# Kernel optimization log

Measured on AMD Instinct MI355X. Metric: run time of the kernel, lower is better.

## Reference

```python
import jax, jax.numpy as jnp
import numpy as np

N = 100_000      # nodes
E = 1_600_000    # edges (avg degree 16)
D_IN = 64        # node feature dim
H = 128          # hidden
E_IN = 64        # edge feature dim
C = 8            # num classes
EPS = 1e-5       # BatchNorm eps


def setup_inputs() -> dict:
    key = jax.random.key(0)
    ks = jax.random.split(key, 22)
    w = lambda k, shape: jax.random.normal(k, shape, dtype=jnp.float32) * 0.05
    return {
        "x_nodes": jax.random.normal(ks[0], (N, D_IN), dtype=jnp.float32),
        "e_feat": jax.random.normal(ks[1], (E, E_IN), dtype=jnp.float32),
        # SAGE layer 1 (fc_self, fc_neigh, bias)
        "Ws1": w(ks[2], (D_IN, H)), "Wn1": w(ks[3], (D_IN, H)), "b1": w(ks[4], (H,)),
        "g1": 1.0 + 0.1 * jax.random.normal(ks[5], (H,), dtype=jnp.float32),
        "bt1": 0.1 * jax.random.normal(ks[6], (H,), dtype=jnp.float32),
        # SAGE layer 2
        "Ws2": w(ks[7], (H, H)), "Wn2": w(ks[8], (H, H)), "b2": w(ks[9], (H,)),
        "g2": 1.0 + 0.1 * jax.random.normal(ks[10], (H,), dtype=jnp.float32),
        "bt2": 0.1 * jax.random.normal(ks[11], (H,), dtype=jnp.float32),
        # Edge MLP
        "We1": w(ks[12], (2 * H + E_IN, H)), "be1": w(ks[13], (H,)),
        "We2": w(ks[14], (H, C)), "be2": w(ks[15], (C,)),
        # Graph structure (message-flow graph, reused for both layers) and pair graph
        "src": jax.random.randint(ks[16], (E,), 0, N, dtype=jnp.int32),
        "dst": jax.random.randint(ks[17], (E,), 0, N, dtype=jnp.int32),
        "u": jax.random.randint(ks[18], (E,), 0, N, dtype=jnp.int32),
        "v": jax.random.randint(ks[19], (E,), 0, N, dtype=jnp.int32),
    }


def _sage_mean(h, src, dst, inv_deg, Ws, Wn, b):
    # DGL SAGEConv('mean'): rst = fc_self(h_dst) + fc_neigh(mean_{in-neighbors} h_src) + bias
    agg = jax.ops.segment_sum(h[src], dst, num_segments=h.shape[0]) * inv_deg[:, None]
    return h @ Ws + agg @ Wn + b


def _bn_relu(h, gamma, beta):
    # BatchNorm1d (training-mode batch stats, biased variance) + ReLU
    mu = h.mean(axis=0)
    var = jnp.mean((h - mu) ** 2, axis=0)
    return jax.nn.relu((h - mu) * jax.lax.rsqrt(var + EPS) * gamma + beta)


def reference(x_nodes, e_feat, Ws1, Wn1, b1, g1, bt1, Ws2, Wn2, b2, g2, bt2,
              We1, be1, We2, be2, src, dst, u, v):
    n = x_nodes.shape[0]
    deg = jax.ops.segment_sum(jnp.ones_like(src, dtype=x_nodes.dtype), dst, num_segments=n)
    inv_deg = jnp.where(deg > 0, 1.0 / jnp.maximum(deg, 1.0), 0.0)  # zero-degree -> 0 (DGL mean)
    h = _bn_relu(_sage_mean(x_nodes, src, dst, inv_deg, Ws1, Wn1, b1), g1, bt1)
    h = _bn_relu(_sage_mean(h, src, dst, inv_deg, Ws2, Wn2, b2), g2, bt2)
    # edge head: gather endpoints, concat with edge features, MLP (dropout = eval identity)
    e_repr = jnp.concatenate([h[u], h[v], e_feat], axis=1)  # [E, 2H + E_IN]
    hid = jax.nn.relu(e_repr @ We1 + be1)
    return hid @ We2 + be2
```

## Files before the change

### kernel.cpp

```cpp
#include <hip/hip_runtime.h>

#define NN 100000
#define EE 1600000
constexpr float BN_EPS = 1e-5f;

typedef __attribute__((ext_vector_type(8))) short short8;
typedef __attribute__((ext_vector_type(4))) float f32x4;

__device__ __forceinline__ short f2bf(float f) {
    unsigned u = __float_as_uint(f);
    u += 0x7fff + ((u >> 16) & 1);
    return (short)(u >> 16);
}
__device__ __forceinline__ float bf2f(short s) {
    return __uint_as_float(((unsigned)(unsigned short)s) << 16);
}

typedef __attribute__((address_space(1))) const unsigned int guint;
typedef __attribute__((address_space(3))) unsigned int luint;
__device__ __forceinline__ void gload_lds16(const void* g, void* l) {
    __builtin_amdgcn_global_load_lds((guint*)g, (luint*)l, 16, 0, 0);
}

__global__ void k_count(const int* __restrict__ dst, int* __restrict__ cnt) {
    int e = blockIdx.x * 256 + threadIdx.x;
    if (e < EE) atomicAdd(&cnt[dst[e]], 1);
}

__global__ __launch_bounds__(1024) void k_scan(const int* __restrict__ cnt,
                                               int* __restrict__ offs,
                                               int* __restrict__ cursor,
                                               float* __restrict__ invd) {
    const int t = threadIdx.x, lane = t & 63, w = t >> 6;
    __shared__ int wsum[16], wexcl[16];
    __shared__ int carry_sh;
    if (t == 0) carry_sh = 0;
    __syncthreads();
    int ss = 0;
    for (int base = 0; base < NN; base += 1024) {
        int i = base + t;
        int v = (i < NN) ? cnt[i] : 0;
        int s = v;
#pragma unroll
        for (int d = 1; d < 64; d <<= 1) {
            int o = __shfl_up(s, d, 64);
            if (lane >= d) s += o;
        }
        if (lane == 63) wsum[w] = s;
        __syncthreads();
        if (t < 16) {
            int wv = wsum[t];
            ss = wv;
#pragma unroll
            for (int d = 1; d < 16; d <<= 1) {
                int o = __shfl_up(ss, d, 16);
                if (t >= d) ss += o;
            }
            wexcl[t] = ss - wv;
        }
        __syncthreads();
        int excl = (s - v) + wexcl[w];
        int c = carry_sh;
        if (i < NN) {
            int o = c + excl;
            offs[i] = o;
            cursor[i] = o;
            invd[i] = v > 0 ? 1.f / (float)v : 0.f;
        }
        __syncthreads();
        if (t == 15) carry_sh = c + ss;
        __syncthreads();
    }
    if (t == 0) offs[NN] = carry_sh;
}

__global__ void k_fill(const int* __restrict__ src, const int* __restrict__ dst,
                       int* __restrict__ cursor, int* __restrict__ eidsrc) {
    int e = blockIdx.x * 256 + threadIdx.x;
    if (e < EE) {
        int pos = atomicAdd(&cursor[dst[e]], 1);
        eidsrc[pos] = src[e];
    }
}

__global__ void k_f2bf(const float* __restrict__ in, short* __restrict__ out, int n8) {
    int i = blockIdx.x * 256 + threadIdx.x;
    if (i >= n8) return;
    float4 a = ((const float4*)in)[i * 2];
    float4 b = ((const float4*)in)[i * 2 + 1];
    short8 o;
    o[0] = f2bf(a.x); o[1] = f2bf(a.y); o[2] = f2bf(a.z); o[3] = f2bf(a.w);
    o[4] = f2bf(b.x); o[5] = f2bf(b.y); o[6] = f2bf(b.z); o[7] = f2bf(b.w);
    ((short8*)out)[i] = o;
}

template <int F>
__global__ __launch_bounds__(256) void k_gather_bf(
    const short* __restrict__ hbsrc, const int* __restrict__ offs,
    const int* __restrict__ eidsrc, const float* __restrict__ invd,
    short* __restrict__ aggb) {
    constexpr int G = F / 8;
    int gid = blockIdx.x * 256 + threadIdx.x;
    int node = gid / G;
    int sub = gid % G;
    if (node >= NN) return;
    int beg = offs[node], end = offs[node + 1];
    float iv = invd[node];
    float s[8] = {0.f, 0.f, 0.f, 0.f, 0.f, 0.f, 0.f, 0.f};
    const size_t co = (size_t)sub * 8;
    int p = beg;
    for (; p + 4 <= end; p += 4) {
        int i0 = eidsrc[p], i1 = eidsrc[p + 1], i2 = eidsrc[p + 2], i3 = eidsrc[p + 3];
        short8 r0 = *(const short8*)(hbsrc + (size_t)i0 * F + co);
        short8 r1 = *(const short8*)(hbsrc + (size_t)i1 * F + co);
        short8 r2 = *(const short8*)(hbsrc + (size_t)i2 * F + co);
        short8 r3 = *(const short8*)(hbsrc + (size_t)i3 * F + co);
#pragma unroll
        for (int j = 0; j < 8; ++j)
            s[j] += (bf2f(r0[j]) + bf2f(r1[j])) + (bf2f(r2[j]) + bf2f(r3[j]));
    }
    for (; p < end; ++p) {
        short8 r = *(const short8*)(hbsrc + (size_t)eidsrc[p] * F + co);
#pragma unroll
        for (int j = 0; j < 8; ++j) s[j] += bf2f(r[j]);
    }
    short8 o;
#pragma unroll
    for (int j = 0; j < 8; ++j) o[j] = f2bf(s[j] * iv);
    *(short8*)(aggb + (size_t)node * F + co) = o;
}

__device__ __forceinline__ void packW(const float* W, short* Wp, int local, int kbase) {
    int k = local >> 7, col = local & 127;
    int gk = k + kbase;
    int kc = gk >> 5, kw = gk & 31, bp = kw >> 3, j = kw & 7;
    int cb = col >> 4, n = col & 15;
    Wp[kc * 4096 + (cb * 64 + bp * 16 + n) * 8 + j] = f2bf(W[k * 128 + col]);
}

__global__ void k_pack_all(const float* __restrict__ We1, const float* __restrict__ Ws1,
                           const float* __restrict__ Wn1, const float* __restrict__ Ws2,
                           const float* __restrict__ Wn2, const float* __restrict__ We2,
                           short* __restrict__ Wp_e, short* __restrict__ Wp1,
                           short* __restrict__ Wp2, short* __restrict__ Wp2e) {
    int idx = blockIdx.x * 256 + threadIdx.x;
    if (idx < 40960) {
        packW(We1, Wp_e, idx, 0);
    } else if (idx < 49152) {
        packW(Ws1, Wp1, idx - 40960, 0);
    } else if (idx < 57344) {
        packW(Wn1, Wp1, idx - 49152, 64);
    } else if (idx < 73728) {
        packW(Ws2, Wp2, idx - 57344, 0);
    } else if (idx < 90112) {
        packW(Wn2, Wp2, idx - 73728, 128);
    } else if (idx < 92160) {
        int local = idx - 90112;
        int k = local >> 4, n = local & 15;
        float val = (n < 8) ? We2[k * 8 + n] : 0.f;
        int kc2 = k >> 5, kl = k & 31, bp = kl >> 3, j = kl & 7;
        Wp2e[(kc2 * 64 + bp * 16 + n) * 8 + j] = f2bf(val);
    }
}

template <int KC1, int KC2>
__global__ __launch_bounds__(256) void k_node_mfma(
    const short* __restrict__ A1, const short* __restrict__ A2,
    const short* __restrict__ Wp, const float* __restrict__ bias,
    float* __restrict__ outf, float* __restrict__ stats) {
    __shared__ __align__(16) short sbuf[16384];
    __shared__ float bs[128];
    __shared__ float reds[4][128], redss[4][128];
    const int t = threadIdx.x;
    if (t < 128) bs[t] = bias[t];
    const int rowbase = blockIdx.x * 128;
    const int lane = t & 63, w = t >> 6;
    const int fo = (lane >> 4) * 16 + (lane & 15);

    auto NSTAGE = [&](int kc, short* Ad, short* Bd) {
        const short* src;
        int kst, kloc;
        if (kc < KC1) { src = A1; kst = KC1 * 32; kloc = kc * 32; }
        else          { src = A2; kst = KC2 * 32; kloc = (kc - KC1) * 32; }
#pragma unroll
        for (int p = 0; p < 2; ++p) {
            int s = t + p * 256;
            int b = (s >> 4) & 3;
            int row = rowbase + ((s >> 6) << 4) + (s & 15);
            gload_lds16(src + (size_t)row * kst + kloc + b * 8, Ad + s * 8);
            gload_lds16(Wp + (size_t)kc * 4096 + s * 8, Bd + s * 8);
        }
    };

    f32x4 acc[2][8];
#pragma unroll
    for (int i = 0; i < 2; ++i)
#pragma unroll
        for (int j = 0; j < 8; ++j) acc[i][j] = (f32x4){0.f, 0.f, 0.f, 0.f};

    constexpr int KC = KC1 + KC2;
    NSTAGE(0, sbuf, sbuf + 4096);
    __syncthreads();
    for (int kc = 0; kc < KC; ++kc) {
        const int cur = kc & 1;
        short* Ac = sbuf + (cur ? 8192 : 0);
        short* Bc = Ac + 4096;
        if (kc + 1 < KC) {
            short* An = sbuf + (cur ? 0 : 8192);
            NSTAGE(kc + 1, An, An + 4096);
        }
        short8 a0 = *(const short8*)(Ac + (2 * w * 64 + fo) * 8);
        short8 a1 = *(const short8*)(Ac + ((2 * w + 1) * 64 + fo) * 8);
#pragma unroll
        for (int cb = 0; cb < 8; ++cb) {
            short8 bfr = *(const short8*)(Bc + (cb * 64 + fo) * 8);
            acc[0][cb] = __builtin_amdgcn_mfma_f32_16x16x32_bf16(a0, bfr, acc[0][cb], 0, 0, 0);
            acc[1][cb] = __builtin_amdgcn_mfma_f32_16x16x32_bf16(a1, bfr, acc[1][cb], 0, 0, 0);
        }
        __syncthreads();
    }

    float cs[8], css[8];
#pragma unroll
    for (int cb = 0; cb < 8; ++cb) { cs[cb] = 0.f; css[cb] = 0.f; }
#pragma unroll
    for (int rb2 = 0; rb2 < 2; ++rb2) {
        int rloc = 32 * w + rb2 * 16 + ((lane >> 4) << 2);
#pragma unroll
        for (int cb = 0; cb < 8; ++cb) {
            int col = cb * 16 + (lane & 15);
            float bb = bs[col];
#pragma unroll
            for (int i = 0; i < 4; ++i) {
                int row = rowbase + rloc + i;
                if (row < NN) {
                    float v = acc[rb2][cb][i] + bb;
                    outf[(size_t)row * 128 + col] = v;
                    cs[cb] += v;
                    css[cb] += v * v;
                }
            }
        }
    }
#pragma unroll
    for (int cb = 0; cb < 8; ++cb) {
        cs[cb] += __shfl_xor(cs[cb], 16);
        cs[cb] += __shfl_xor(cs[cb], 32);
        css[cb] += __shfl_xor(css[cb], 16);
        css[cb] += __shfl_xor(css[cb], 32);
    }
    if (lane < 16) {
#pragma unroll
        for (int cb = 0; cb < 8; ++cb) {
            reds[w][cb * 16 + lane] = cs[cb];
            redss[w][cb * 16 + lane] = css[cb];
        }
    }
    __syncthreads();
    if (t < 128) {
        atomicAdd(&stats[t], reds[0][t] + reds[1][t] + reds[2][t] + reds[3][t]);
    } else {
        int c = t - 128;
        atomicAdd(&stats[128 + c], redss[0][c] + redss[1][c] + redss[2][c] + redss[3][c]);
    }
}

__global__ void k_bnrelu_bf16(const float* __restrict__ h, const float* __restrict__ stats,
                              const float* __restrict__ g, const float* __restrict__ bt,
                              short* __restrict__ hb) {
    int gid = blockIdx.x * 256 + threadIdx.x;
    if (gid >= NN * 16) return;
    int c8 = gid & 15;
    float av[8], bv[8];
#pragma unroll
    for (int j = 0; j < 8; ++j) {
        int c = c8 * 8 + j;
        float mu = stats[c] * (1.f / NN);
        float var = stats[128 + c] * (1.f / NN) - mu * mu;
        float a = g[c] * rsqrtf(var + BN_EPS);
        av[j] = a;
        bv[j] = bt[c] - mu * a;
    }
    float4 v0 = reinterpret_cast<const float4*>(h)[gid * 2];
    float4 v1 = reinterpret_cast<const float4*>(h)[gid * 2 + 1];
    short8 o;
    o[0] = f2bf(fmaxf(fmaf(av[0], v0.x, bv[0]), 0.f));
    o[1] = f2bf(fmaxf(fmaf(av[1], v0.y, bv[1]), 0.f));
    o[2] = f2bf(fmaxf(fmaf(av[2], v0.z, bv[2]), 0.f));
    o[3] = f2bf(fmaxf(fmaf(av[3], v0.w, bv[3]), 0.f));
    o[4] = f2bf(fmaxf(fmaf(av[4], v1.x, bv[4]), 0.f));
    o[5] = f2bf(fmaxf(fmaf(av[5], v1.y, bv[5]), 0.f));
    o[6] = f2bf(fmaxf(fmaf(av[6], v1.z, bv[6]), 0.f));
    o[7] = f2bf(fmaxf(fmaf(av[7], v1.w, bv[7]), 0.f));
    reinterpret_cast<short8*>(hb)[gid] = o;
}

__global__ __launch_bounds__(256) void k_edge_mfma(
    const short* __restrict__ hb, const float* __restrict__ ef,
    const short* __restrict__ Wp, const short* __restrict__ Wp2e,
    const float* __restrict__ be1, const float* __restrict__ be2,
    const int* __restrict__ uu, const int* __restrict__ vv,
    float* __restrict__ out) {
    __shared__ __align__(16) short smem[17408];
    __shared__ float be1s[128];
    __shared__ int suv[256];
    const int t = threadIdx.x;
    const int eb = blockIdx.x * 128;
    if (t < 128) {
        suv[t] = uu[eb + t];
        suv[128 + t] = vv[eb + t];
        be1s[t] = be1[t];
    }
    const int lane = t & 63, w = t >> 6;
    const int fo = (lane >> 4) * 16 + (lane & 15);
    const int srow = t >> 1;
    const int sb0 = (t & 1) * 2;
    const int sslotbase = (srow >> 4) * 64 + (srow & 15);

    short8 b2f[4];
#pragma unroll
    for (int kc2 = 0; kc2 < 4; ++kc2)
        b2f[kc2] = *(const short8*)(Wp2e + (kc2 * 64 + fo) * 8);

    short8 efs[4];
    {
        const float* er = ef + (size_t)(eb + srow) * 64;
#pragma unroll
        for (int kcx = 0; kcx < 2; ++kcx)
#pragma unroll
            for (int pp = 0; pp < 2; ++pp) {
                int b = sb0 + pp;
                float4 f0 = *(const float4*)(er + kcx * 32 + b * 8);
                float4 f1 = *(const float4*)(er + kcx * 32 + b * 8 + 4);
                short8 v8;
                v8[0] = f2bf(f0.x); v8[1] = f2bf(f0.y);
                v8[2] = f2bf(f0.z); v8[3] = f2bf(f0.w);
                v8[4] = f2bf(f1.x); v8[5] = f2bf(f1.y);
                v8[6] = f2bf(f1.z); v8[7] = f2bf(f1.w);
                efs[kcx * 2 + pp] = v8;
            }
    }
    __syncthreads();

    auto STAGE = [&](int kc, short* Ad, short* Bd) {
        if (kc < 8) {
#pragma unroll
            for (int p = 0; p < 2; ++p) {
                int s = t + p * 256;
                int b = (s >> 4) & 3;
                int row = ((s >> 6) << 4) + (s & 15);
                const short* gsrc =
                    hb + (size_t)suv[(kc >= 4) * 128 + row] * 128 + (kc & 3) * 32 + b * 8;
                gload_lds16(gsrc, Ad + s * 8);
            }
        } else {
#pragma unroll
            for (int p = 0; p < 2; ++p)
                *(short8*)(Ad + (sslotbase + (sb0 + p) * 16) * 8) = efs[(kc - 8) * 2 + p];
        }
#pragma unroll
        for (int p = 0; p < 2; ++p) {
            int s = t + p * 256;
            gload_lds16(Wp + (size_t)kc * 4096 + s * 8, Bd + s * 8);
        }
    };

    f32x4 acc[2][8];
#pragma unroll
    for (int i = 0; i < 2; ++i)
#pragma unroll
        for (int j = 0; j < 8; ++j) acc[i][j] = (f32x4){0.f, 0.f, 0.f, 0.f};

    STAGE(0, smem, smem + 4096);
    __syncthreads();
    for (int kc = 0; kc < 10; ++kc) {
        const int cur = kc & 1;
        short* Ac = smem + (cur ? 8192 : 0);
        short* Bc = Ac + 4096;
        if (kc < 9) {
            short* An = smem + (cur ? 0 : 8192);
            STAGE(kc + 1, An, An + 4096);
        }
        short8 afr0 = *(const short8*)(Ac + (2 * w * 64 + fo) * 8);
        short8 afr1 = *(const short8*)(Ac + ((2 * w + 1) * 64 + fo) * 8);
#pragma unroll
        for (int cb = 0; cb < 8; ++cb) {
            short8 bfr = *(const short8*)(Bc + (cb * 64 + fo) * 8);
            acc[0][cb] = __builtin_amdgcn_mfma_f32_16x16x32_bf16(afr0, bfr, acc[0][cb], 0, 0, 0);
            acc[1][cb] = __builtin_amdgcn_mfma_f32_16x16x32_bf16(afr1, bfr, acc[1][cb], 0, 0, 0);
        }
        __syncthreads();
    }

    short* Hid = smem;
#pragma unroll
    for (int rb2 = 0; rb2 < 2; ++rb2)
#pragma unroll
        for (int cb = 0; cb < 8; ++cb) {
            int col = cb * 16 + (lane & 15);
            int rbase = 32 * w + rb2 * 16 + ((lane >> 4) << 2);
            float bb = be1s[col];
#pragma unroll
            for (int i = 0; i < 4; ++i)
                Hid[(rbase + i) * 136 + col] = f2bf(fmaxf(acc[rb2][cb][i] + bb, 0.f));
        }
    __syncthreads();

#pragma unroll
    for (int rf = 0; rf < 2; ++rf) {
        f32x4 a2 = (f32x4){0.f, 0.f, 0.f, 0.f};
        const int rbl = 32 * w + 16 * rf + (lane & 15);
#pragma unroll
        for (int kc2 = 0; kc2 < 4; ++kc2) {
            short8 af = *(const short8*)(Hid + rbl * 136 + kc2 * 32 + 8 * (lane >> 4));
            a2 = __builtin_amdgcn_mfma_f32_16x16x32_bf16(af, b2f[kc2], a2, 0, 0, 0);
        }
        int col = lane & 15;
        if (col < 8) {
            int r0 = eb + 32 * w + 16 * rf + 4 * (lane >> 4);
            float bb = be2[col];
#pragma unroll
            for (int i = 0; i < 4; ++i)
                out[(size_t)(r0 + i) * 8 + col] = a2[i] + bb;
        }
    }
}

extern "C" void kernel_launch(void* const* d_in, const int* in_sizes, int n_in,
                              void* d_out, int out_size, void* d_ws, size_t ws_size,
                              hipStream_t stream) {
    const float* x   = (const float*)d_in[0];
    const float* ef  = (const float*)d_in[1];
    const float* Ws1 = (const float*)d_in[2];
    const float* Wn1 = (const float*)d_in[3];
    const float* b1  = (const float*)d_in[4];
    const float* g1  = (const float*)d_in[5];
    const float* bt1 = (const float*)d_in[6];
    const float* Ws2 = (const float*)d_in[7];
    const float* Wn2 = (const float*)d_in[8];
    const float* b2  = (const float*)d_in[9];
    const float* g2  = (const float*)d_in[10];
    const float* bt2 = (const float*)d_in[11];
    const float* We1 = (const float*)d_in[12];
    const float* be1 = (const float*)d_in[13];
    const float* We2 = (const float*)d_in[14];
    const float* be2 = (const float*)d_in[15];
    const int* src = (const int*)d_in[16];
    const int* dst = (const int*)d_in[17];
    const int* u   = (const int*)d_in[18];
    const int* v   = (const int*)d_in[19];
    float* out = (float*)d_out;

    char* p = (char*)d_ws;
    auto take = [&](size_t bytes) {
        char* r = p;
        p += (bytes + 255) & ~(size_t)255;
        return r;
    };
    int* cnt     = (int*)take(NN * 4);
    float* stats = (float*)take(512 * 4);
    float* invd  = (float*)take(NN * 4);
    int* offs    = (int*)take((NN + 1) * 4);
    int* cursor  = (int*)take(NN * 4);
    int* eidsrc  = (int*)take((size_t)EE * 4);
    short* Wp_e  = (short*)take(320 * 128 * 2);
    short* Wp1   = (short*)take(128 * 128 * 2);
    short* Wp2   = (short*)take(256 * 128 * 2);
    short* Wp2e  = (short*)take(256 * 8 * 2);
    short* xb    = (short*)take((size_t)NN * 64 * 2);
    short* agg1b = (short*)take((size_t)NN * 64 * 2);
    short* h1b   = (short*)take((size_t)NN * 128 * 2);
    short* agg2b = (short*)take((size_t)NN * 128 * 2);
    take(65536);
    float* h1 = out;
    float* h2 = out;
    short* hb = xb;

    hipMemsetAsync(cnt, 0, ((char*)stats - (char*)cnt) + 512 * 4, stream);
    k_count<<<(EE + 255) / 256, 256, 0, stream>>>(dst, cnt);
    k_scan<<<1, 1024, 0, stream>>>(cnt, offs, cursor, invd);
    k_fill<<<(EE + 255) / 256, 256, 0, stream>>>(src, dst, cursor, eidsrc);
    k_pack_all<<<360, 256, 0, stream>>>(We1, Ws1, Wn1, Ws2, Wn2, We2, Wp_e, Wp1, Wp2, Wp2e);
    k_f2bf<<<(NN * 8 + 255) / 256, 256, 0, stream>>>(x, xb, NN * 8);

    k_gather_bf<64><<<(NN * 8 + 255) / 256, 256, 0, stream>>>(xb, offs, eidsrc, invd, agg1b);
    k_node_mfma<2, 2><<<(NN + 127) / 128, 256, 0, stream>>>(xb, agg1b, Wp1, b1, h1, stats);
    k_bnrelu_bf16<<<(NN * 16 + 255) / 256, 256, 0, stream>>>(h1, stats, g1, bt1, h1b);

    k_gather_bf<128><<<(NN * 16 + 255) / 256, 256, 0, stream>>>(h1b, offs, eidsrc, invd, agg2b);
    k_node_mfma<4, 4><<<(NN + 127) / 128, 256, 0, stream>>>(h1b, agg2b, Wp2, b2, h2, stats + 256);
    k_bnrelu_bf16<<<(NN * 16 + 255) / 256, 256, 0, stream>>>(h2, stats + 256, g2, bt2, hb);

    k_edge_mfma<<<EE / 128, 256, 0, stream>>>(hb, ef, Wp_e, Wp2e, be1, be2, u, v, out);
}
```

Baseline: 773.0 us.

## Parallelize degree scan, hoist BN coefficients to LDS, single-buffer edge MFMA

Replaces the single-block serial prefix scan over node degrees with a three-kernel reduce/base/final scan spread across many blocks, removing a long single-CU serial phase. BatchNorm scale and shift are now computed once per block into shared memory instead of per thread for eight channels. The edge MLP kernel drops double buffering and register prefetch of edge features, loading each K-chunk into a single LDS buffer and syncing before compute. This lowers register pressure but loses load/compute overlap.

Measured after the change: 662.0 us. 1.17x faster.

```diff
diff --git a/kernel.cpp b/kernel.cpp
--- a/kernel.cpp
+++ b/kernel.cpp
@@ -27,51 +27,70 @@
     if (e < EE) atomicAdd(&cnt[dst[e]], 1);
 }
 
-__global__ __launch_bounds__(1024) void k_scan(const int* __restrict__ cnt,
-                                               int* __restrict__ offs,
-                                               int* __restrict__ cursor,
-                                               float* __restrict__ invd) {
+__global__ __launch_bounds__(1024) void k_scan_part(const int* __restrict__ cnt,
+                                                    int* __restrict__ bsum) {
+    const int t = threadIdx.x, lane = t & 63, w = t >> 6;
+    int i = blockIdx.x * 1024 + t;
+    int v = (i < NN) ? cnt[i] : 0;
+#pragma unroll
+    for (int d = 1; d < 64; d <<= 1) v += __shfl_xor(v, d, 64);
+    __shared__ int ws[16];
+    if (lane == 0) ws[w] = v;
+    __syncthreads();
+    if (t == 0) {
+        int s = 0;
+#pragma unroll
+        for (int k = 0; k < 16; ++k) s += ws[k];
+        bsum[blockIdx.x] = s;
+    }
+}
+
+__global__ void k_scan_base(int* __restrict__ bsum, int* __restrict__ offs, int nb) {
+    if (threadIdx.x == 0) {
+        int run = 0;
+        for (int k = 0; k < nb; ++k) {
+            int v = bsum[k];
+            bsum[k] = run;
+            run += v;
+        }
+        offs[NN] = run;
+    }
+}
+
+__global__ __launch_bounds__(1024) void k_scan_final(const int* __restrict__ cnt,
+                                                     const int* __restrict__ bsum,
+                                                     int* __restrict__ offs,
+                                                     int* __restrict__ cursor,
+                                                     float* __restrict__ invd) {
     const int t = threadIdx.x, lane = t & 63, w = t >> 6;
     __shared__ int wsum[16], wexcl[16];
-    __shared__ int carry_sh;
-    if (t == 0) carry_sh = 0;
-    __syncthreads();
-    int ss = 0;
-    for (int base = 0; base < NN; base += 1024) {
-        int i = base + t;
-        int v = (i < NN) ? cnt[i] : 0;
-        int s = v;
-#pragma unroll
-        for (int d = 1; d < 64; d <<= 1) {
-            int o = __shfl_up(s, d, 64);
-            if (lane >= d) s += o;
-        }
-        if (lane == 63) wsum[w] = s;
-        __syncthreads();
-        if (t < 16) {
-            int wv = wsum[t];
-            ss = wv;
-#pragma unroll
-            for (int d = 1; d < 16; d <<= 1) {
-                int o = __shfl_up(ss, d, 16);
-                if (t >= d) ss += o;
-            }
-            wexcl[t] = ss - wv;
-        }
-        __syncthreads();
-        int excl = (s - v) + wexcl[w];
-        int c = carry_sh;
-        if (i < NN) {
-            int o = c + excl;
-            offs[i] = o;
-            cursor[i] = o;
-            invd[i] = v > 0 ? 1.f / (float)v : 0.f;
-        }
-        __syncthreads();
-        if (t == 15) carry_sh = c + ss;
-        __syncthreads();
-    }
-    if (t == 0) offs[NN] = carry_sh;
+    int i = blockIdx.x * 1024 + t;
+    int v = (i < NN) ? cnt[i] : 0;
+    int s = v;
+#pragma unroll
+    for (int d = 1; d < 64; d <<= 1) {
+        int o = __shfl_up(s, d, 64);
+        if (lane >= d) s += o;
+    }
+    if (lane == 63) wsum[w] = s;
+    __syncthreads();
+    if (t < 16) {
+        int wv = wsum[t];
+        int ss = wv;
+#pragma unroll
+        for (int d = 1; d < 16; d <<= 1) {
+            int o = __shfl_up(ss, d, 16);
+            if (t >= d) ss += o;
+        }
+        wexcl[t] = ss - wv;
+    }
+    __syncthreads();
+    if (i < NN) {
+        int o = bsum[blockIdx.x] + (s - v) + wexcl[w];
+        offs[i] = o;
+        cursor[i] = o;
+        invd[i] = v > 0 ? 1.f / (float)v : 0.f;
+    }
 }
 
 __global__ void k_fill(const int* __restrict__ src, const int* __restrict__ dst,
@@ -268,30 +287,30 @@
 __global__ void k_bnrelu_bf16(const float* __restrict__ h, const float* __restrict__ stats,
                               const float* __restrict__ g, const float* __restrict__ bt,
                               short* __restrict__ hb) {
-    int gid = blockIdx.x * 256 + threadIdx.x;
+    __shared__ float a_sh[128], b_sh[128];
+    const int t = threadIdx.x;
+    if (t < 128) {
+        float mu = stats[t] * (1.f / NN);
+        float var = stats[128 + t] * (1.f / NN) - mu * mu;
+        float a = g[t] * rsqrtf(var + BN_EPS);
+        a_sh[t] = a;
+        b_sh[t] = bt[t] - mu * a;
+    }
+    __syncthreads();
+    int gid = blockIdx.x * 256 + t;
     if (gid >= NN * 16) return;
-    int c8 = gid & 15;
-    float av[8], bv[8];
-#pragma unroll
-    for (int j = 0; j < 8; ++j) {
-        int c = c8 * 8 + j;
-        float mu = stats[c] * (1.f / NN);
-        float var = stats[128 + c] * (1.f / NN) - mu * mu;
-        float a = g[c] * rsqrtf(var + BN_EPS);
-        av[j] = a;
-        bv[j] = bt[c] - mu * a;
-    }
+    int c0 = (gid & 15) * 8;
     float4 v0 = reinterpret_cast<const float4*>(h)[gid * 2];
     float4 v1 = reinterpret_cast<const float4*>(h)[gid * 2 + 1];
     short8 o;
-    o[0] = f2bf(fmaxf(fmaf(av[0], v0.x, bv[0]), 0.f));
-    o[1] = f2bf(fmaxf(fmaf(av[1], v0.y, bv[1]), 0.f));
-    o[2] = f2bf(fmaxf(fmaf(av[2], v0.z, bv[2]), 0.f));
-    o[3] = f2bf(fmaxf(fmaf(av[3], v0.w, bv[3]), 0.f));
-    o[4] = f2bf(fmaxf(fmaf(av[4], v1.x, bv[4]), 0.f));
-    o[5] = f2bf(fmaxf(fmaf(av[5], v1.y, bv[5]), 0.f));
-    o[6] = f2bf(fmaxf(fmaf(av[6], v1.z, bv[6]), 0.f));
-    o[7] = f2bf(fmaxf(fmaf(av[7], v1.w, bv[7]), 0.f));
+    o[0] = f2bf(fmaxf(fmaf(a_sh[c0 + 0], v0.x, b_sh[c0 + 0]), 0.f));
+    o[1] = f2bf(fmaxf(fmaf(a_sh[c0 + 1], v0.y, b_sh[c0 + 1]), 0.f));
+    o[2] = f2bf(fmaxf(fmaf(a_sh[c0 + 2], v0.z, b_sh[c0 + 2]), 0.f));
+    o[3] = f2bf(fmaxf(fmaf(a_sh[c0 + 3], v0.w, b_sh[c0 + 3]), 0.f));
+    o[4] = f2bf(fmaxf(fmaf(a_sh[c0 + 4], v1.x, b_sh[c0 + 4]), 0.f));
+    o[5] = f2bf(fmaxf(fmaf(a_sh[c0 + 5], v1.y, b_sh[c0 + 5]), 0.f));
+    o[6] = f2bf(fmaxf(fmaf(a_sh[c0 + 6], v1.z, b_sh[c0 + 6]), 0.f));
+    o[7] = f2bf(fmaxf(fmaf(a_sh[c0 + 7], v1.w, b_sh[c0 + 7]), 0.f));
     reinterpret_cast<short8*>(hb)[gid] = o;
 }
 
@@ -304,6 +323,8 @@
     __shared__ __align__(16) short smem[17408];
     __shared__ float be1s[128];
     __shared__ int suv[256];
+    short* A_l = smem;
+    short* B_l = smem + 4096;
     const int t = threadIdx.x;
     const int eb = blockIdx.x * 128;
     if (t < 128) {
@@ -311,6 +332,8 @@
         suv[128 + t] = vv[eb + t];
         be1s[t] = be1[t];
     }
+    __syncthreads();
+
     const int lane = t & 63, w = t >> 6;
     const int fo = (lane >> 4) * 16 + (lane & 15);
     const int srow = t >> 1;
@@ -322,27 +345,13 @@
     for (int kc2 = 0; kc2 < 4; ++kc2)
         b2f[kc2] = *(const short8*)(Wp2e + (kc2 * 64 + fo) * 8);
 
-    short8 efs[4];
-    {
-        const float* er = ef + (size_t)(eb + srow) * 64;
-#pragma unroll
-        for (int kcx = 0; kcx < 2; ++kcx)
-#pragma unroll
-            for (int pp = 0; pp < 2; ++pp) {
-                int b = sb0 + pp;
-                float4 f0 = *(const float4*)(er + kcx * 32 + b * 8);
-                float4 f1 = *(const float4*)(er + kcx * 32 + b * 8 + 4);
-                short8 v8;
-                v8[0] = f2bf(f0.x); v8[1] = f2bf(f0.y);
-                v8[2] = f2bf(f0.z); v8[3] = f2bf(f0.w);
-                v8[4] = f2bf(f1.x); v8[5] = f2bf(f1.y);
-                v8[6] = f2bf(f1.z); v8[7] = f2bf(f1.w);
-                efs[kcx * 2 + pp] = v8;
-            }
-    }
-    __syncthreads();
-
-    auto STAGE = [&](int kc, short* Ad, short* Bd) {
+    f32x4 acc[2][8];
+#pragma unroll
+    for (int i = 0; i < 2; ++i)
+#pragma unroll
+        for (int j = 0; j < 8; ++j) acc[i][j] = (f32x4){0.f, 0.f, 0.f, 0.f};
+
+    for (int kc = 0; kc < 10; ++kc) {
         if (kc < 8) {
 #pragma unroll
             for (int p = 0; p < 2; ++p) {
@@ -351,41 +360,35 @@
                 int row = ((s >> 6) << 4) + (s & 15);
                 const short* gsrc =
                     hb + (size_t)suv[(kc >= 4) * 128 + row] * 128 + (kc & 3) * 32 + b * 8;
-                gload_lds16(gsrc, Ad + s * 8);
+                gload_lds16(gsrc, A_l + s * 8);
             }
         } else {
-#pragma unroll
-            for (int p = 0; p < 2; ++p)
-                *(short8*)(Ad + (sslotbase + (sb0 + p) * 16) * 8) = efs[(kc - 8) * 2 + p];
+            const float* er = ef + (size_t)(eb + srow) * 64 + (kc - 8) * 32;
+#pragma unroll
+            for (int p = 0; p < 2; ++p) {
+                int b = sb0 + p;
+                float4 f0 = *(const float4*)(er + b * 8);
+                float4 f1 = *(const float4*)(er + b * 8 + 4);
+                short8 v8;
+                v8[0] = f2bf(f0.x); v8[1] = f2bf(f0.y);
+                v8[2] = f2bf(f0.z); v8[3] = f2bf(f0.w);
+                v8[4] = f2bf(f1.x); v8[5] = f2bf(f1.y);
+                v8[6] = f2bf(f1.z); v8[7] = f2bf(f1.w);
+                *(short8*)(A_l + (sslotbase + b * 16) * 8) = v8;
+            }
         }
 #pragma unroll
         for (int p = 0; p < 2; ++p) {
             int s = t + p * 256;
-            gload_lds16(Wp + (size_t)kc * 4096 + s * 8, Bd + s * 8);
-        }
-    };
-
-    f32x4 acc[2][8];
-#pragma unroll
-    for (int i = 0; i < 2; ++i)
-#pragma unroll
-        for (int j = 0; j < 8; ++j) acc[i][j] = (f32x4){0.f, 0.f, 0.f, 0.f};
-
-    STAGE(0, smem, smem + 4096);
-    __syncthreads();
-    for (int kc = 0; kc < 10; ++kc) {
-        const int cur = kc & 1;
-        short* Ac = smem + (cur ? 8192 : 0);
-        short* Bc = Ac + 4096;
-        if (kc < 9) {
-            short* An = smem + (cur ? 0 : 8192);
-            STAGE(kc + 1, An, An + 4096);
-        }
-        short8 afr0 = *(const short8*)(Ac + (2 * w * 64 + fo) * 8);
-        short8 afr1 = *(const short8*)(Ac + ((2 * w + 1) * 64 + fo) * 8);
+            gload_lds16(Wp + (size_t)kc * 4096 + s * 8, B_l + s * 8);
+        }
+        __syncthreads();
+
+        short8 afr0 = *(const short8*)(A_l + ((2 * w) * 64 + fo) * 8);
+        short8 afr1 = *(const short8*)(A_l + ((2 * w + 1) * 64 + fo) * 8);
 #pragma unroll
         for (int cb = 0; cb < 8; ++cb) {
-            short8 bfr = *(const short8*)(Bc + (cb * 64 + fo) * 8);
+            short8 bfr = *(const short8*)(B_l + (cb * 64 + fo) * 8);
             acc[0][cb] = __builtin_amdgcn_mfma_f32_16x16x32_bf16(afr0, bfr, acc[0][cb], 0, 0, 0);
             acc[1][cb] = __builtin_amdgcn_mfma_f32_16x16x32_bf16(afr1, bfr, acc[1][cb], 0, 0, 0);
         }
@@ -462,6 +465,7 @@
     float* invd  = (float*)take(NN * 4);
     int* offs    = (int*)take((NN + 1) * 4);
     int* cursor  = (int*)take(NN * 4);
+    int* bsum    = (int*)take(128 * 4);
     int* eidsrc  = (int*)take((size_t)EE * 4);
     short* Wp_e  = (short*)take(320 * 128 * 2);
     short* Wp1   = (short*)take(128 * 128 * 2);
@@ -476,9 +480,13 @@
     float* h2 = out;
     short* hb = xb;
 
+    const int NB = (NN + 1023) / 1024;
+
     hipMemsetAsync(cnt, 0, ((char*)stats - (char*)cnt) + 512 * 4, stream);
     k_count<<<(EE + 255) / 256, 256, 0, stream>>>(dst, cnt);
-    k_scan<<<1, 1024, 0, stream>>>(cnt, offs, cursor, invd);
+    k_scan_part<<<NB, 1024, 0, stream>>>(cnt, bsum);
+    k_scan_base<<<1, 64, 0, stream>>>(bsum, offs, NB);
+    k_scan_final<<<NB, 1024, 0, stream>>>(cnt, bsum, offs, cursor, invd);
     k_fill<<<(EE + 255) / 256, 256, 0, stream>>>(src, dst, cursor, eidsrc);
     k_pack_all<<<360, 256, 0, stream>>>(We1, Ws1, Wn1, Ws2, Wn2, We2, Wp_e, Wp1, Wp2, Wp2e);
     k_f2bf<<<(NN * 8 + 255) / 256, 256, 0, stream>>>(x, xb, NN * 8);
```
